# Optimization experiments

Hardware: AMD Instinct MI355X
Metric: run time of the kernel (lower is better)

## Reference

```python
import jax, jax.numpy as jnp
import numpy as np

D_MODEL = 768
N_HEADS = 12
HEAD_DIM = D_MODEL // N_HEADS
B, L = 2, 4096


def setup_inputs() -> dict:
    key = jax.random.key(0)
    ks = jax.random.split(key, 11)
    s = 0.02
    inp = {
        "q": jax.random.normal(ks[0], (B, L, D_MODEL), jnp.float32),
        "k": jax.random.normal(ks[1], (B, L, D_MODEL), jnp.float32),
        "v": jax.random.normal(ks[2], (B, L, D_MODEL), jnp.float32),
        # causal mask: True = masked (matches torch masked_fill semantics)
        "mask": jnp.triu(jnp.ones((L, L), bool), k=1)[None, None, :, :],
        "wq": jax.random.normal(ks[3], (D_MODEL, D_MODEL), jnp.float32) * s,
        "bq": jnp.zeros((D_MODEL,), jnp.float32),
        "wk": jax.random.normal(ks[4], (D_MODEL, D_MODEL), jnp.float32) * s,
        "bk": jnp.zeros((D_MODEL,), jnp.float32),
        "wv": jax.random.normal(ks[5], (D_MODEL, D_MODEL), jnp.float32) * s,
        "bv": jnp.zeros((D_MODEL,), jnp.float32),
        "wo": jax.random.normal(ks[6], (D_MODEL, D_MODEL), jnp.float32) * s,
        "bo": jnp.zeros((D_MODEL,), jnp.float32),
    }
    return inp


def reference(q, k, v, mask, wq, bq, wk, bk, wv, bv, wo, bo):
    Bs, Ls, Ds = q.shape

    def split_heads(x):  # [B,L,D] -> [B,H,L,hd]
        return x.reshape(Bs, -1, N_HEADS, HEAD_DIM).transpose(0, 2, 1, 3)

    qh = split_heads(q @ wq.T + bq)
    kh = split_heads(k @ wk.T + bk)
    vh = split_heads(v @ wv.T + bv)

    scores = jnp.einsum("bhqd,bhkd->bhqk", qh, kh) / jnp.sqrt(
        jnp.asarray(HEAD_DIM, qh.dtype)
    )
    scores = jnp.where(mask, -jnp.inf, scores)
    attn = jax.nn.softmax(scores, axis=-1)
    out = jnp.einsum("bhqk,bhkd->bhqd", attn, vh)  # [B,H,L,hd]
    out = out.transpose(0, 2, 1, 3).reshape(Bs, Ls, Ds)
    return out @ wo.T + bo
```

## Files before the change

kernel.cpp:

```cpp
#include <hip/hip_runtime.h>
#include <hip/hip_bf16.h>
#include <stdint.h>

#define DM 768
#define NH 12
#define HD 64
#define BB 2
#define LL 4096
#define BH (BB*NH)
#define ML (BB*LL)

typedef short bf16x8 __attribute__((ext_vector_type(8)));
typedef short bf16x4 __attribute__((ext_vector_type(4)));
typedef float f32x4 __attribute__((ext_vector_type(4)));

__device__ inline short f2b(float f) {
  __hip_bfloat16 h = __float2bfloat16(f);
  return *reinterpret_cast<short*>(&h);
}

__device__ inline void gll16(const void* g, void* l) {
  __builtin_amdgcn_global_load_lds(
      (const __attribute__((address_space(1))) unsigned int*)g,
      (__attribute__((address_space(3))) unsigned int*)l, 16, 0, 0);
}

__global__ __launch_bounds__(256) void convx_kernel(
    const float* __restrict__ src, short* __restrict__ dst)
{
  size_t i = ((size_t)blockIdx.x * 256 + threadIdx.x) * 8;
  float4 a = *(const float4*)(src + i);
  float4 b = *(const float4*)(src + i + 4);
  bf16x8 r = {f2b(a.x), f2b(a.y), f2b(a.z), f2b(a.w),
              f2b(b.x), f2b(b.y), f2b(b.z), f2b(b.w)};
  *(bf16x8*)(dst + i) = r;
}

__global__ __launch_bounds__(256) void convw_kernel(
    const float* __restrict__ w0, const float* __restrict__ w1,
    const float* __restrict__ w2, const float* __restrict__ w3,
    short* __restrict__ o0, short* __restrict__ o1,
    short* __restrict__ o2, short* __restrict__ o3)
{
  const float* src; short* dst;
  switch (blockIdx.y) {
    case 0: src = w0; dst = o0; break;
    case 1: src = w1; dst = o1; break;
    case 2: src = w2; dst = o2; break;
    default: src = w3; dst = o3; break;
  }
  size_t i = ((size_t)blockIdx.x * 256 + threadIdx.x) * 8;
  float4 a = *(const float4*)(src + i);
  float4 b = *(const float4*)(src + i + 4);
  bf16x8 r = {f2b(a.x), f2b(a.y), f2b(a.z), f2b(a.w),
              f2b(b.x), f2b(b.y), f2b(b.z), f2b(b.w)};
  *(bf16x8*)(dst + i) = r;
}

template<int MODE>
__global__ __launch_bounds__(256) void gemm_kernel(
    const short* __restrict__ A, const short* __restrict__ Bw,
    const float* __restrict__ bias, void* __restrict__ outp, float scale)
{
  __shared__ __align__(16) short abuf[2][128 * 64];
  __shared__ __align__(16) short bbuf[2][64 * 64];

  const int lane = threadIdx.x & 63;
  const int w    = threadIdx.x >> 6;
  const int g    = lane >> 4;
  const int mr   = lane & 15;
  const int wr   = w >> 1;
  const int wc   = w & 1;
  const int m0   = blockIdx.x * 128;
  const int n0   = blockIdx.y * 64;

  const int srow = lane >> 3;
  const int scol = ((lane & 7) ^ srow) * 8;

  #pragma unroll
  for (int i = 0; i < 4; ++i)
    gll16(A + (size_t)(m0 + w * 32 + i * 8 + srow) * DM + scol,
          (char*)abuf[0] + (w * 32 + i * 8) * 128);
  #pragma unroll
  for (int i = 0; i < 2; ++i)
    gll16(Bw + (size_t)(n0 + w * 16 + i * 8 + srow) * DM + scol,
          (char*)bbuf[0] + (w * 16 + i * 8) * 128);

  f32x4 acc[4][2] = {};
  const int nk = DM / 64;
  for (int t = 0; t < nk; ++t) {
    __syncthreads();
    if (t + 1 < nk) {
      const int k1 = (t + 1) * 64;
      #pragma unroll
      for (int i = 0; i < 4; ++i)
        gll16(A + (size_t)(m0 + w * 32 + i * 8 + srow) * DM + k1 + scol,
              (char*)abuf[(t + 1) & 1] + (w * 32 + i * 8) * 128);
      #pragma unroll
      for (int i = 0; i < 2; ++i)
        gll16(Bw + (size_t)(n0 + w * 16 + i * 8 + srow) * DM + k1 + scol,
              (char*)bbuf[(t + 1) & 1] + (w * 16 + i * 8) * 128);
    }
    const char* ab = (const char*)abuf[t & 1];
    const char* bb = (const char*)bbuf[t & 1];
    #pragma unroll
    for (int ks = 0; ks < 2; ++ks) {
      const int chunk = ((ks * 4 + g) ^ (mr & 7)) * 16;
      bf16x8 af[4], bfr[2];
      #pragma unroll
      for (int m = 0; m < 4; ++m)
        af[m] = *(const bf16x8*)(ab + (wr * 64 + m * 16 + mr) * 128 + chunk);
      #pragma unroll
      for (int nf = 0; nf < 2; ++nf)
        bfr[nf] = *(const bf16x8*)(bb + (wc * 32 + nf * 16 + mr) * 128 + chunk);
      #pragma unroll
      for (int m = 0; m < 4; ++m)
        #pragma unroll
        for (int nf = 0; nf < 2; ++nf)
          acc[m][nf] = __builtin_amdgcn_mfma_f32_16x16x32_bf16(af[m], bfr[nf], acc[m][nf], 0, 0, 0);
    }
  }

  #pragma unroll
  for (int nf = 0; nf < 2; ++nf) {
    const int col = n0 + wc * 32 + nf * 16 + mr;
    const float bv = bias[col];
    if (MODE == 3) {
      float* out = (float*)outp;
      #pragma unroll
      for (int m = 0; m < 4; ++m)
        #pragma unroll
        for (int r = 0; r < 4; ++r) {
          const int row = m0 + wr * 64 + m * 16 + g * 4 + r;
          out[(size_t)row * DM + col] = acc[m][nf][r] + bv;
        }
    } else {
      short* out = (short*)outp;
      const int h = col >> 6, c = col & 63;
      #pragma unroll
      for (int m = 0; m < 4; ++m)
        #pragma unroll
        for (int r = 0; r < 4; ++r) {
          const int row = m0 + wr * 64 + m * 16 + g * 4 + r;
          const int b = row >> 12, li = row & 4095;
          const float val = (acc[m][nf][r] + bv) * scale;
          size_t idx;
          if (MODE == 2) idx = ((size_t)(b * NH + h) * HD + c) * LL + li;
          else           idx = ((size_t)(b * NH + h) * LL + li) * HD + c;
          out[idx] = f2b(val);
        }
    }
  }
}

__global__ __launch_bounds__(256) void attn_kernel(
    const short* __restrict__ qh, const short* __restrict__ kh,
    const short* __restrict__ vt, short* __restrict__ attn_out)
{
  __shared__ __align__(16) char kbuf[2][8192];
  __shared__ __align__(16) char vbuf[2][8192];
  __shared__ __align__(16) char plds[4][2048];

  const int bh    = blockIdx.y;
  const int lane  = threadIdx.x & 63;
  const int w     = threadIdx.x >> 6;
  const int g     = lane >> 4;
  const int mr    = lane & 15;
  const int q0blk = ((int)gridDim.x - 1 - (int)blockIdx.x) * 64;
  const int q0w   = q0blk + w * 16;
  const int nt    = q0blk / 64 + 1;

  const short* qp = qh + (size_t)bh * LL * HD;
  const short* kp = kh + (size_t)bh * LL * HD;
  const short* vp = vt + (size_t)bh * HD * LL;
  char* wbase = plds[w];

  const short* qrow = qp + (size_t)(q0w + mr) * HD + g * 8;
  bf16x8 qb0 = *(const bf16x8*)qrow;
  bf16x8 qb1 = *(const bf16x8*)(qrow + 32);

  f32x4 acc[4] = {};
  float lreg = 0.f;

  int wroff[4], rdoff[2];
  #pragma unroll
  for (int mf = 0; mf < 4; ++mf)
    wroff[mf] = mr * 128 + ((mf * 32 + g * 8) ^ ((mr & 7) << 4));
  #pragma unroll
  for (int c = 0; c < 2; ++c)
    rdoff[c] = mr * 128 + ((c * 64 + g * 16) ^ ((mr & 7) << 4));
  const int swz = (mr & 7) << 4;
  const int ssub = lane >> 3;
  const int scol = ((lane & 7) ^ ssub) * 8;

  #pragma unroll
  for (int p = 0; p < 2; ++p) {
    const int row = p * 32 + w * 8 + ssub;
    gll16(kp + (size_t)row * HD + scol, kbuf[0] + p * 4096 + w * 1024);
    gll16(vp + (size_t)row * LL + scol, vbuf[0] + p * 4096 + w * 1024);
  }

  for (int t = 0; t < nt; ++t) {
    __syncthreads();
    const int kv0 = t * 64;

    if (t + 1 < nt) {
      const int kv1 = kv0 + 64;
      char* kb = kbuf[(t + 1) & 1];
      char* vb = vbuf[(t + 1) & 1];
      #pragma unroll
      for (int p = 0; p < 2; ++p) {
        const int row = p * 32 + w * 8 + ssub;
        gll16(kp + (size_t)(kv1 + row) * HD + scol, kb + p * 4096 + w * 1024);
        gll16(vp + (size_t)row * LL + kv1 + scol, vb + p * 4096 + w * 1024);
      }
    }

    if (kv0 < q0w + 16) {
      const char* kb = kbuf[t & 1];
      const char* vb = vbuf[t & 1];

      f32x4 s[4] = {};
      #pragma unroll
      for (int mf = 0; mf < 4; ++mf) {
        const char* krow = kb + (mf * 16 + mr) * 128;
        bf16x8 ka0 = *(const bf16x8*)(krow + ((g * 16) ^ swz));
        bf16x8 ka1 = *(const bf16x8*)(krow + ((64 + g * 16) ^ swz));
        s[mf] = __builtin_amdgcn_mfma_f32_16x16x32_bf16(ka0, qb0, s[mf], 0, 0, 0);
        s[mf] = __builtin_amdgcn_mfma_f32_16x16x32_bf16(ka1, qb1, s[mf], 0, 0, 0);
      }

      if (kv0 + 63 > q0w) {
        #pragma unroll
        for (int mf = 0; mf < 4; ++mf)
          #pragma unroll
          for (int r = 0; r < 4; ++r)
            if (kv0 + mf * 16 + g * 4 + r > q0w + mr)
              s[mf][r] = -INFINITY;
      }

      float sa[4];
      #pragma unroll
      for (int mf = 0; mf < 4; ++mf) {
        #pragma unroll
        for (int r = 0; r < 4; ++r)
          s[mf][r] = __expf(s[mf][r]);
        sa[mf] = (s[mf][0] + s[mf][1]) + (s[mf][2] + s[mf][3]);
      }
      float rs = (sa[0] + sa[1]) + (sa[2] + sa[3]);
      rs += __shfl_xor(rs, 16, 64);
      rs += __shfl_xor(rs, 32, 64);
      lreg += rs;

      #pragma unroll
      for (int mf = 0; mf < 4; ++mf) {
        bf16x4 w4 = {f2b(s[mf][0]), f2b(s[mf][1]), f2b(s[mf][2]), f2b(s[mf][3])};
        *(bf16x4*)(wbase + wroff[mf]) = w4;
      }

      #pragma unroll
      for (int c = 0; c < 2; ++c) {
        bf16x8 pb = *(const bf16x8*)(wbase + rdoff[c]);
        #pragma unroll
        for (int df = 0; df < 4; ++df) {
          const char* vrow = vb + (df * 16 + mr) * 128;
          bf16x8 av = *(const bf16x8*)(vrow + ((c * 64 + g * 16) ^ swz));
          acc[df] = __builtin_amdgcn_mfma_f32_16x16x32_bf16(av, pb, acc[df], 0, 0, 0);
        }
      }
    }
  }

  const int b = bh / NH, h = bh % NH;
  const float inv = 1.0f / lreg;
  const int q = q0w + mr;
  short* orow = attn_out + ((size_t)(b * LL + q)) * DM + h * HD + g * 4;
  #pragma unroll
  for (int df = 0; df < 4; ++df) {
    bf16x4 st = {f2b(acc[df][0] * inv), f2b(acc[df][1] * inv),
                 f2b(acc[df][2] * inv), f2b(acc[df][3] * inv)};
    *(bf16x4*)(orow + df * 16) = st;
  }
}

extern "C" void kernel_launch(void* const* d_in, const int* in_sizes, int n_in,
                              void* d_out, int out_size, void* d_ws, size_t ws_size,
                              hipStream_t stream) {
  const float* q  = (const float*)d_in[0];
  const float* k  = (const float*)d_in[1];
  const float* v  = (const float*)d_in[2];
  const float* wq = (const float*)d_in[4];
  const float* bq = (const float*)d_in[5];
  const float* wk = (const float*)d_in[6];
  const float* bk = (const float*)d_in[7];
  const float* wv = (const float*)d_in[8];
  const float* bv = (const float*)d_in[9];
  const float* wo = (const float*)d_in[10];
  const float* bo = (const float*)d_in[11];

  const size_t S   = (size_t)BH * LL * HD;
  const size_t WSZ = (size_t)DM * DM;
  short* qh   = (short*)d_ws;
  short* kh   = qh + S;
  short* vt   = kh + S;
  short* attn = vt + S;
  short* wqb  = attn + S;
  short* wkb  = wqb + WSZ;
  short* wvb  = wkb + WSZ;
  short* wob  = wvb + WSZ;
  short* xb   = attn;

  dim3 blk(256);
  convw_kernel<<<dim3(WSZ / 2048, 4), blk, 0, stream>>>(wq, wk, wv, wo, wqb, wkb, wvb, wob);
  dim3 ggemm(ML / 128, DM / 64);
  convx_kernel<<<dim3((ML * DM) / 2048), blk, 0, stream>>>(q, xb);
  gemm_kernel<0><<<ggemm, blk, 0, stream>>>(xb, wqb, bq, qh, 0.125f);
  convx_kernel<<<dim3((ML * DM) / 2048), blk, 0, stream>>>(k, xb);
  gemm_kernel<1><<<ggemm, blk, 0, stream>>>(xb, wkb, bk, kh, 1.0f);
  convx_kernel<<<dim3((ML * DM) / 2048), blk, 0, stream>>>(v, xb);
  gemm_kernel<2><<<ggemm, blk, 0, stream>>>(xb, wvb, bv, vt, 1.0f);

  attn_kernel<<<dim3(LL / 64, BH), blk, 0, stream>>>(qh, kh, vt, attn);
  gemm_kernel<3><<<ggemm, blk, 0, stream>>>(attn, wob, bo, d_out, 1.0f);
}
```

Measured before the change: 398.3 us.

## Batch QKV projections into one launch and pair causal attention tiles per block

Converts q/k/v to bf16 in a single launch and runs all three projection GEMMs in one grid with a z dimension, when the workspace is large enough. The attention kernel now gives each block two query tiles, one long and one short, so every block does roughly equal causal work and the grid has half as many blocks. Softmax uses exp2 with log2(e) folded into the Q scale. The aim is fewer launches, more blocks in flight during the projections, and less tail imbalance in attention, at the cost of extra workspace and a fallback path when that workspace is unavailable.

```diff
diff --git a/kernel.cpp b/kernel.cpp
--- a/kernel.cpp
+++ b/kernel.cpp
@@ -14,6 +14,8 @@
 typedef short bf16x4 __attribute__((ext_vector_type(4)));
 typedef float f32x4 __attribute__((ext_vector_type(4)));
 
+#define LOG2E 1.4426950408889634f
+
 __device__ inline short f2b(float f) {
   __hip_bfloat16 h = __float2bfloat16(f);
   return *reinterpret_cast<short*>(&h);
@@ -36,6 +38,21 @@
   *(bf16x8*)(dst + i) = r;
 }
 
+__global__ __launch_bounds__(256) void convx3_kernel(
+    const float* __restrict__ s0, const float* __restrict__ s1,
+    const float* __restrict__ s2, short* __restrict__ d0,
+    short* __restrict__ d1, short* __restrict__ d2)
+{
+  const float* src = blockIdx.y == 0 ? s0 : (blockIdx.y == 1 ? s1 : s2);
+  short*       dst = blockIdx.y == 0 ? d0 : (blockIdx.y == 1 ? d1 : d2);
+  size_t i = ((size_t)blockIdx.x * 256 + threadIdx.x) * 8;
+  float4 a = *(const float4*)(src + i);
+  float4 b = *(const float4*)(src + i + 4);
+  bf16x8 r = {f2b(a.x), f2b(a.y), f2b(a.z), f2b(a.w),
+              f2b(b.x), f2b(b.y), f2b(b.z), f2b(b.w)};
+  *(bf16x8*)(dst + i) = r;
+}
+
 __global__ __launch_bounds__(256) void convw_kernel(
     const float* __restrict__ w0, const float* __restrict__ w1,
     const float* __restrict__ w2, const float* __restrict__ w3,
@@ -57,25 +74,24 @@
   *(bf16x8*)(dst + i) = r;
 }
 
-template<int MODE>
-__global__ __launch_bounds__(256) void gemm_kernel(
+struct GemmAcc { f32x4 a[4][2]; };
+
+__device__ inline void gemm_core(
     const short* __restrict__ A, const short* __restrict__ Bw,
-    const float* __restrict__ bias, void* __restrict__ outp, float scale)
-{
-  __shared__ __align__(16) short abuf[2][128 * 64];
-  __shared__ __align__(16) short bbuf[2][64 * 64];
-
+    int m0, int n0, short* abuf0, short* abuf1, short* bbuf0, short* bbuf1,
+    GemmAcc& G)
+{
   const int lane = threadIdx.x & 63;
   const int w    = threadIdx.x >> 6;
   const int g    = lane >> 4;
   const int mr   = lane & 15;
   const int wr   = w >> 1;
   const int wc   = w & 1;
-  const int m0   = blockIdx.x * 128;
-  const int n0   = blockIdx.y * 64;
-
   const int srow = lane >> 3;
   const int scol = ((lane & 7) ^ srow) * 8;
+
+  short* abuf[2] = {abuf0, abuf1};
+  short* bbuf[2] = {bbuf0, bbuf1};
 
   #pragma unroll
   for (int i = 0; i < 4; ++i)
@@ -86,7 +102,6 @@
     gll16(Bw + (size_t)(n0 + w * 16 + i * 8 + srow) * DM + scol,
           (char*)bbuf[0] + (w * 16 + i * 8) * 128);
 
-  f32x4 acc[4][2] = {};
   const int nk = DM / 64;
   for (int t = 0; t < nk; ++t) {
     __syncthreads();
@@ -117,39 +132,107 @@
       for (int m = 0; m < 4; ++m)
         #pragma unroll
         for (int nf = 0; nf < 2; ++nf)
-          acc[m][nf] = __builtin_amdgcn_mfma_f32_16x16x32_bf16(af[m], bfr[nf], acc[m][nf], 0, 0, 0);
+          G.a[m][nf] = __builtin_amdgcn_mfma_f32_16x16x32_bf16(af[m], bfr[nf], G.a[m][nf], 0, 0, 0);
     }
   }
-
+}
+
+__device__ inline void gemm_epi_bf16(
+    GemmAcc& G, const float* __restrict__ bias, short* __restrict__ out,
+    int m0, int n0, float scale, bool vmode)
+{
+  const int lane = threadIdx.x & 63;
+  const int w    = threadIdx.x >> 6;
+  const int g    = lane >> 4;
+  const int mr   = lane & 15;
+  const int wr   = w >> 1;
+  const int wc   = w & 1;
   #pragma unroll
   for (int nf = 0; nf < 2; ++nf) {
     const int col = n0 + wc * 32 + nf * 16 + mr;
     const float bv = bias[col];
-    if (MODE == 3) {
-      float* out = (float*)outp;
-      #pragma unroll
-      for (int m = 0; m < 4; ++m)
-        #pragma unroll
-        for (int r = 0; r < 4; ++r) {
-          const int row = m0 + wr * 64 + m * 16 + g * 4 + r;
-          out[(size_t)row * DM + col] = acc[m][nf][r] + bv;
-        }
-    } else {
-      short* out = (short*)outp;
-      const int h = col >> 6, c = col & 63;
-      #pragma unroll
-      for (int m = 0; m < 4; ++m)
-        #pragma unroll
-        for (int r = 0; r < 4; ++r) {
-          const int row = m0 + wr * 64 + m * 16 + g * 4 + r;
-          const int b = row >> 12, li = row & 4095;
-          const float val = (acc[m][nf][r] + bv) * scale;
-          size_t idx;
-          if (MODE == 2) idx = ((size_t)(b * NH + h) * HD + c) * LL + li;
-          else           idx = ((size_t)(b * NH + h) * LL + li) * HD + c;
-          out[idx] = f2b(val);
-        }
-    }
+    const int h = col >> 6, c = col & 63;
+    #pragma unroll
+    for (int m = 0; m < 4; ++m)
+      #pragma unroll
+      for (int r = 0; r < 4; ++r) {
+        const int row = m0 + wr * 64 + m * 16 + g * 4 + r;
+        const int b = row >> 12, li = row & 4095;
+        const float val = (G.a[m][nf][r] + bv) * scale;
+        size_t idx;
+        if (vmode) idx = ((size_t)(b * NH + h) * HD + c) * LL + li;
+        else       idx = ((size_t)(b * NH + h) * LL + li) * HD + c;
+        out[idx] = f2b(val);
+      }
+  }
+}
+
+__global__ __launch_bounds__(256) void qkv_gemm_kernel(
+    const short* __restrict__ xq, const short* __restrict__ xk,
+    const short* __restrict__ xv, const short* __restrict__ wqb,
+    const short* __restrict__ wkb, const short* __restrict__ wvb,
+    const float* __restrict__ bq, const float* __restrict__ bk,
+    const float* __restrict__ bv, short* __restrict__ qh,
+    short* __restrict__ kh, short* __restrict__ vt)
+{
+  __shared__ __align__(16) short abuf[2][128 * 64];
+  __shared__ __align__(16) short bbuf[2][64 * 64];
+  const int z = blockIdx.z;
+  const short* A  = z == 0 ? xq : (z == 1 ? xk : xv);
+  const short* Bw = z == 0 ? wqb : (z == 1 ? wkb : wvb);
+  const float* bi = z == 0 ? bq : (z == 1 ? bk : bv);
+  short* out      = z == 0 ? qh : (z == 1 ? kh : vt);
+  const float scale = z == 0 ? 0.125f * LOG2E : 1.0f;
+  const int m0 = blockIdx.x * 128;
+  const int n0 = blockIdx.y * 64;
+
+  GemmAcc G = {};
+  gemm_core(A, Bw, m0, n0, abuf[0], abuf[1], bbuf[0], bbuf[1], G);
+  gemm_epi_bf16(G, bi, out, m0, n0, scale, z == 2);
+}
+
+template<int MODE>
+__global__ __launch_bounds__(256) void proj_gemm_kernel(
+    const short* __restrict__ A, const short* __restrict__ Bw,
+    const float* __restrict__ bias, short* __restrict__ out, float scale)
+{
+  __shared__ __align__(16) short abuf[2][128 * 64];
+  __shared__ __align__(16) short bbuf[2][64 * 64];
+  const int m0 = blockIdx.x * 128;
+  const int n0 = blockIdx.y * 64;
+  GemmAcc G = {};
+  gemm_core(A, Bw, m0, n0, abuf[0], abuf[1], bbuf[0], bbuf[1], G);
+  gemm_epi_bf16(G, bias, out, m0, n0, scale, MODE == 2);
+}
+
+__global__ __launch_bounds__(256) void outproj_kernel(
+    const short* __restrict__ A, const short* __restrict__ Bw,
+    const float* __restrict__ bias, float* __restrict__ out)
+{
+  __shared__ __align__(16) short abuf[2][128 * 64];
+  __shared__ __align__(16) short bbuf[2][64 * 64];
+  const int m0 = blockIdx.x * 128;
+  const int n0 = blockIdx.y * 64;
+  GemmAcc G = {};
+  gemm_core(A, Bw, m0, n0, abuf[0], abuf[1], bbuf[0], bbuf[1], G);
+
+  const int lane = threadIdx.x & 63;
+  const int w    = threadIdx.x >> 6;
+  const int g    = lane >> 4;
+  const int mr   = lane & 15;
+  const int wr   = w >> 1;
+  const int wc   = w & 1;
+  #pragma unroll
+  for (int nf = 0; nf < 2; ++nf) {
+    const int col = n0 + wc * 32 + nf * 16 + mr;
+    const float bv = bias[col];
+    #pragma unroll
+    for (int m = 0; m < 4; ++m)
+      #pragma unroll
+      for (int r = 0; r < 4; ++r) {
+        const int row = m0 + wr * 64 + m * 16 + g * 4 + r;
+        out[(size_t)row * DM + col] = G.a[m][nf][r] + bv;
+      }
   }
 }
 
@@ -161,26 +244,16 @@
   __shared__ __align__(16) char vbuf[2][8192];
   __shared__ __align__(16) char plds[4][2048];
 
-  const int bh    = blockIdx.y;
-  const int lane  = threadIdx.x & 63;
-  const int w     = threadIdx.x >> 6;
-  const int g     = lane >> 4;
-  const int mr    = lane & 15;
-  const int q0blk = ((int)gridDim.x - 1 - (int)blockIdx.x) * 64;
-  const int q0w   = q0blk + w * 16;
-  const int nt    = q0blk / 64 + 1;
+  const int bh   = blockIdx.y;
+  const int lane = threadIdx.x & 63;
+  const int w    = threadIdx.x >> 6;
+  const int g    = lane >> 4;
+  const int mr   = lane & 15;
 
   const short* qp = qh + (size_t)bh * LL * HD;
   const short* kp = kh + (size_t)bh * LL * HD;
   const short* vp = vt + (size_t)bh * HD * LL;
   char* wbase = plds[w];
-
-  const short* qrow = qp + (size_t)(q0w + mr) * HD + g * 8;
-  bf16x8 qb0 = *(const bf16x8*)qrow;
-  bf16x8 qb1 = *(const bf16x8*)(qrow + 32);
-
-  f32x4 acc[4] = {};
-  float lreg = 0.f;
 
   int wroff[4], rdoff[2];
   #pragma unroll
@@ -193,93 +266,111 @@
   const int ssub = lane >> 3;
   const int scol = ((lane & 7) ^ ssub) * 8;
 
-  #pragma unroll
-  for (int p = 0; p < 2; ++p) {
-    const int row = p * 32 + w * 8 + ssub;
-    gll16(kp + (size_t)row * HD + scol, kbuf[0] + p * 4096 + w * 1024);
-    gll16(vp + (size_t)row * LL + scol, vbuf[0] + p * 4096 + w * 1024);
-  }
-
-  for (int t = 0; t < nt; ++t) {
-    __syncthreads();
-    const int kv0 = t * 64;
-
-    if (t + 1 < nt) {
-      const int kv1 = kv0 + 64;
-      char* kb = kbuf[(t + 1) & 1];
-      char* vb = vbuf[(t + 1) & 1];
-      #pragma unroll
-      for (int p = 0; p < 2; ++p) {
-        const int row = p * 32 + w * 8 + ssub;
-        gll16(kp + (size_t)(kv1 + row) * HD + scol, kb + p * 4096 + w * 1024);
-        gll16(vp + (size_t)row * LL + kv1 + scol, vb + p * 4096 + w * 1024);
+  const int b = bh / NH, h = bh % NH;
+
+  #pragma unroll
+  for (int ph = 0; ph < 2; ++ph) {
+    const int qtile = ph == 0 ? (63 - (int)blockIdx.x) : (int)blockIdx.x;
+    const int q0blk = qtile * 64;
+    const int q0w   = q0blk + w * 16;
+    const int nt    = qtile + 1;
+
+    if (ph == 1) __syncthreads();
+
+    const short* qrow = qp + (size_t)(q0w + mr) * HD + g * 8;
+    bf16x8 qb0 = *(const bf16x8*)qrow;
+    bf16x8 qb1 = *(const bf16x8*)(qrow + 32);
+
+    f32x4 acc[4] = {};
+    float lreg = 0.f;
+
+    #pragma unroll
+    for (int p = 0; p < 2; ++p) {
+      const int row = p * 32 + w * 8 + ssub;
+      gll16(kp + (size_t)row * HD + scol, kbuf[0] + p * 4096 + w * 1024);
+      gll16(vp + (size_t)row * LL + scol, vbuf[0] + p * 4096 + w * 1024);
+    }
+
+    for (int t = 0; t < nt; ++t) {
+      __syncthreads();
+      const int kv0 = t * 64;
+
+      if (t + 1 < nt) {
+        const int kv1 = kv0 + 64;
+        char* kb = kbuf[(t + 1) & 1];
+        char* vb = vbuf[(t + 1) & 1];
+        #pragma unroll
+        for (int p = 0; p < 2; ++p) {
+          const int row = p * 32 + w * 8 + ssub;
+          gll16(kp + (size_t)(kv1 + row) * HD + scol, kb + p * 4096 + w * 1024);
+          gll16(vp + (size_t)row * LL + kv1 + scol, vb + p * 4096 + w * 1024);
+        }
+      }
+
+      {
+        const char* kb = kbuf[t & 1];
+        const char* vb = vbuf[t & 1];
+
+        f32x4 s[4] = {};
+        #pragma unroll
+        for (int mf = 0; mf < 4; ++mf) {
+          const char* krow = kb + (mf * 16 + mr) * 128;
+          bf16x8 ka0 = *(const bf16x8*)(krow + ((g * 16) ^ swz));
+          bf16x8 ka1 = *(const bf16x8*)(krow + ((64 + g * 16) ^ swz));
+          s[mf] = __builtin_amdgcn_mfma_f32_16x16x32_bf16(ka0, qb0, s[mf], 0, 0, 0);
+          s[mf] = __builtin_amdgcn_mfma_f32_16x16x32_bf16(ka1, qb1, s[mf], 0, 0, 0);
+        }
+
+        if (kv0 + 63 > q0w) {
+          #pragma unroll
+          for (int mf = 0; mf < 4; ++mf)
+            #pragma unroll
+            for (int r = 0; r < 4; ++r)
+              if (kv0 + mf * 16 + g * 4 + r > q0w + mr)
+                s[mf][r] = -INFINITY;
+        }
+
+        float sa[4];
+        #pragma unroll
+        for (int mf = 0; mf < 4; ++mf) {
+          #pragma unroll
+          for (int r = 0; r < 4; ++r)
+            s[mf][r] = exp2f(s[mf][r]);
+          sa[mf] = (s[mf][0] + s[mf][1]) + (s[mf][2] + s[mf][3]);
+        }
+        float rs = (sa[0] + sa[1]) + (sa[2] + sa[3]);
+        rs += __shfl_xor(rs, 16, 64);
+        rs += __shfl_xor(rs, 32, 64);
+        lreg += rs;
+
+        #pragma unroll
+        for (int mf = 0; mf < 4; ++mf) {
+          bf16x4 w4 = {f2b(s[mf][0]), f2b(s[mf][1]), f2b(s[mf][2]), f2b(s[mf][3])};
+          *(bf16x4*)(wbase + wroff[mf]) = w4;
+        }
+
+        #pragma unroll
+        for (int c = 0; c < 2; ++c) {
+          bf16x8 pb = *(const bf16x8*)(wbase + rdoff[c]);
+          #pragma unroll
+          for (int df = 0; df < 4; ++df) {
+            const char* vrow = vb + (df * 16 + mr) * 128;
+            bf16x8 av = *(const bf16x8*)(vrow + ((c * 64 + g * 16) ^ swz));
+            acc[df] = __builtin_amdgcn_mfma_f32_16x16x32_bf16(av, pb, acc[df], 0, 0, 0);
+          }
+        }
       }
     }
 
-    if (kv0 < q0w + 16) {
-      const char* kb = kbuf[t & 1];
-      const char* vb = vbuf[t & 1];
-
-      f32x4 s[4] = {};
-      #pragma unroll
-      for (int mf = 0; mf < 4; ++mf) {
-        const char* krow = kb + (mf * 16 + mr) * 128;
-        bf16x8 ka0 = *(const bf16x8*)(krow + ((g * 16) ^ swz));
-        bf16x8 ka1 = *(const bf16x8*)(krow + ((64 + g * 16) ^ swz));
-        s[mf] = __builtin_amdgcn_mfma_f32_16x16x32_bf16(ka0, qb0, s[mf], 0, 0, 0);
-        s[mf] = __builtin_amdgcn_mfma_f32_16x16x32_bf16(ka1, qb1, s[mf], 0, 0, 0);
-      }
-
-      if (kv0 + 63 > q0w) {
-        #pragma unroll
-        for (int mf = 0; mf < 4; ++mf)
-          #pragma unroll
-          for (int r = 0; r < 4; ++r)
-            if (kv0 + mf * 16 + g * 4 + r > q0w + mr)
-              s[mf][r] = -INFINITY;
-      }
-
-      float sa[4];
-      #pragma unroll
-      for (int mf = 0; mf < 4; ++mf) {
-        #pragma unroll
-        for (int r = 0; r < 4; ++r)
-          s[mf][r] = __expf(s[mf][r]);
-        sa[mf] = (s[mf][0] + s[mf][1]) + (s[mf][2] + s[mf][3]);
-      }
-      float rs = (sa[0] + sa[1]) + (sa[2] + sa[3]);
-      rs += __shfl_xor(rs, 16, 64);
-      rs += __shfl_xor(rs, 32, 64);
-      lreg += rs;
-
-      #pragma unroll
-      for (int mf = 0; mf < 4; ++mf) {
-        bf16x4 w4 = {f2b(s[mf][0]), f2b(s[mf][1]), f2b(s[mf][2]), f2b(s[mf][3])};
-        *(bf16x4*)(wbase + wroff[mf]) = w4;
-      }
-
-      #pragma unroll
-      for (int c = 0; c < 2; ++c) {
-        bf16x8 pb = *(const bf16x8*)(wbase + rdoff[c]);
-        #pragma unroll
-        for (int df = 0; df < 4; ++df) {
-          const char* vrow = vb + (df * 16 + mr) * 128;
-          bf16x8 av = *(const bf16x8*)(vrow + ((c * 64 + g * 16) ^ swz));
-          acc[df] = __builtin_amdgcn_mfma_f32_16x16x32_bf16(av, pb, acc[df], 0, 0, 0);
-        }
-      }
+    const float inv = 1.0f / lreg;
+    const int q = q0w + mr;
+    short* orow = attn_out + ((size_t)(b * LL + q)) * DM + h * HD + g * 4;
+    #pragma unroll
+    for (int df = 0; df < 4; ++df) {
+      bf16x4 st = {f2b(acc[df][0] * inv), f2b(acc[df][1] * inv),
+                   f2b(acc[df][2] * inv), f2b(acc[df][3] * inv)};
+      *(bf16x4*)(orow + df * 16) = st;
     }
-  }
-
-  const int b = bh / NH, h = bh % NH;
-  const float inv = 1.0f / lreg;
-  const int q = q0w + mr;
-  short* orow = attn_out + ((size_t)(b * LL + q)) * DM + h * HD + g * 4;
-  #pragma unroll
-  for (int df = 0; df < 4; ++df) {
-    bf16x4 st = {f2b(acc[df][0] * inv), f2b(acc[df][1] * inv),
-                 f2b(acc[df][2] * inv), f2b(acc[df][3] * inv)};
-    *(bf16x4*)(orow + df * 16) = st;
   }
 }
 
@@ -308,18 +399,32 @@
   short* wkb  = wqb + WSZ;
   short* wvb  = wkb + WSZ;
   short* wob  = wvb + WSZ;
-  short* xb   = attn;
+  short* xtra = wob + WSZ;
+
+  const size_t need_fused = (size_t)(6 * S + 4 * WSZ) * sizeof(short);
+  const bool fused = ws_size >= need_fused;
 
   dim3 blk(256);
   convw_kernel<<<dim3(WSZ / 2048, 4), blk, 0, stream>>>(wq, wk, wv, wo, wqb, wkb, wvb, wob);
   dim3 ggemm(ML / 128, DM / 64);
-  convx_kernel<<<dim3((ML * DM) / 2048), blk, 0, stream>>>(q, xb);
-  gemm_kernel<0><<<ggemm, blk, 0, stream>>>(xb, wqb, bq, qh, 0.125f);
-  convx_kernel<<<dim3((ML * DM) / 2048), blk, 0, stream>>>(k, xb);
-  gemm_kernel<1><<<ggemm, blk, 0, stream>>>(xb, wkb, bk, kh, 1.0f);
-  convx_kernel<<<dim3((ML * DM) / 2048), blk, 0, stream>>>(v, xb);
-  gemm_kernel<2><<<ggemm, blk, 0, stream>>>(xb, wvb, bv, vt, 1.0f);
-
-  attn_kernel<<<dim3(LL / 64, BH), blk, 0, stream>>>(qh, kh, vt, attn);
-  gemm_kernel<3><<<ggemm, blk, 0, stream>>>(attn, wob, bo, d_out, 1.0f);
-}
+
+  if (fused) {
+    short* xbq = attn;
+    short* xbk = xtra;
+    short* xbv = xtra + S;
+    convx3_kernel<<<dim3(S / 2048, 3), blk, 0, stream>>>(q, k, v, xbq, xbk, xbv);
+    qkv_gemm_kernel<<<dim3(ML / 128, DM / 64, 3), blk, 0, stream>>>(
+        xbq, xbk, xbv, wqb, wkb, wvb, bq, bk, bv, qh, kh, vt);
+  } else {
+    short* xb = attn;
+    convx_kernel<<<dim3(S / 2048), blk, 0, stream>>>(q, xb);
+    proj_gemm_kernel<0><<<ggemm, blk, 0, stream>>>(xb, wqb, bq, qh, 0.125f * LOG2E);
+    convx_kernel<<<dim3(S / 2048), blk, 0, stream>>>(k, xb);
+    proj_gemm_kernel<1><<<ggemm, blk, 0, stream>>>(xb, wkb, bk, kh, 1.0f);
+    convx_kernel<<<dim3(S / 2048), blk, 0, stream>>>(v, xb);
+    proj_gemm_kernel<2><<<ggemm, blk, 0, stream>>>(xb, wvb, bv, vt, 1.0f);
+  }
+
+  attn_kernel<<<dim3(32, BH), blk, 0, stream>>>(qh, kh, vt, attn);
+  outproj_kernel<<<ggemm, blk, 0, stream>>>(attn, wob, bo, (float*)d_out);
+}
```

After: 382.1 us. 4.1% less time.
